# Optimization experiments

Measured on AMD Instinct MI355X. Metric: run time of the kernel, lower is better.

Reference implementation:

```python
import jax, jax.numpy as jnp
import numpy as np

D_MODEL = 1024
D_FF = 4096
N_EXPERTS = 8
TOP_K = 2

def setup_inputs() -> dict:
    key = jax.random.key(0)
    ks = jax.random.split(key, 8)
    s = 1.0 / np.sqrt(D_MODEL)
    sf = 1.0 / np.sqrt(D_FF)
    return {
        "x": jax.random.normal(ks[0], (4, 1024, D_MODEL), dtype=jnp.float32),
        "W1": jax.random.uniform(ks[1], (N_EXPERTS, D_MODEL, D_FF), jnp.float32, -s, s),
        "b1": jax.random.uniform(ks[2], (N_EXPERTS, D_FF), jnp.float32, -s, s),
        "W2": jax.random.uniform(ks[3], (N_EXPERTS, D_FF, D_MODEL), jnp.float32, -sf, sf),
        "b2": jax.random.uniform(ks[4], (N_EXPERTS, D_MODEL), jnp.float32, -sf, sf),
        "Wg": jax.random.uniform(ks[5], (D_MODEL, N_EXPERTS), jnp.float32, -s, s),
        "bg": jax.random.uniform(ks[6], (N_EXPERTS,), jnp.float32, -s, s),
    }

def reference(x, W1, b1, W2, b2, Wg, bg):
    # gate: [B,S,E]
    logits = jnp.einsum('bsd,de->bse', x, Wg) + bg
    probs = jax.nn.softmax(logits, axis=-1)
    # top-k mask + renormalize (k < n_experts)
    topk_vals, topk_idx = jax.lax.top_k(probs, TOP_K)
    mask = jax.nn.one_hot(topk_idx, N_EXPERTS, dtype=probs.dtype).sum(axis=-2)
    probs = probs * mask
    denom = probs.sum(axis=-1, keepdims=True)
    denom = denom + (denom == 0).astype(probs.dtype)
    probs = probs / denom
    # dense expert compute: all experts on all tokens. h: [B,E,S,d_ff]
    h = jnp.einsum('bsd,edf->besf', x, W1) + b1[None, :, None, :]
    h = jax.nn.gelu(h, approximate=False)
    y = jnp.einsum('besf,efd->besd', h, W2) + b2[None, :, None, :]
    # weighted combine over experts: [B,S,d]
    out = jnp.einsum('bse,besd->bsd', probs, y)
    return out
```

## Files before the change

### kernel.cpp

```cpp
#include <hip/hip_runtime.h>
#include <hip/hip_bf16.h>

#define NTOK   4096
#define DMODEL 1024
#define DFF    4096
#define NEXP   8
#define TOPK   2
#define BM 128
#define BN 128
#define BK 64
#define NSLOT   (NTOK*TOPK)
#define MAXSLOT (NSLOT + NEXP*BM)
#define MAXTILE (MAXSLOT/BM)

typedef __attribute__((ext_vector_type(8))) short bf16x8;
typedef __attribute__((ext_vector_type(8))) unsigned short u16x8;
typedef __attribute__((ext_vector_type(4))) float f32x4;

__device__ __forceinline__ unsigned short f2bf(float f){
    union { float f; unsigned int u; } v; v.f = f;
    unsigned int r = (v.u + 0x7fffu + ((v.u >> 16) & 1u)) >> 16;
    return (unsigned short)r;
}

__device__ __forceinline__ void gload16(const unsigned short* g, unsigned short* l){
    __builtin_amdgcn_global_load_lds(
        (const __attribute__((address_space(1))) void*)g,
        (__attribute__((address_space(3))) void*)l,
        16, 0, 0);
}

__global__ __launch_bounds__(256) void k_transpose_convert2(const float* __restrict__ W1,
                                                            const float* __restrict__ W2,
                                                            unsigned short* __restrict__ W1t,
                                                            unsigned short* __restrict__ W2t)
{
    __shared__ float tile[64][65];
    int z = blockIdx.z;
    const float* src; unsigned short* dst; int R, C, r0, c0;
    if(z < 8){
        src = W1  + (size_t)z * DMODEL * DFF;
        dst = W1t + (size_t)z * DMODEL * DFF;
        R = DMODEL; C = DFF;
        r0 = blockIdx.y * 64; c0 = blockIdx.x * 64;
    } else {
        src = W2  + (size_t)(z-8) * DFF * DMODEL;
        dst = W2t + (size_t)(z-8) * DFF * DMODEL;
        R = DFF; C = DMODEL;
        r0 = blockIdx.x * 64; c0 = blockIdx.y * 64;
    }
    int t = threadIdx.x;
    int tr  = t >> 4;
    int tc4 = (t & 15) * 4;
    #pragma unroll
    for(int i=0;i<4;i++){
        float4 v = *(const float4*)&src[(size_t)(r0 + tr + i*16)*C + c0 + tc4];
        tile[tc4+0][tr + i*16] = v.x;
        tile[tc4+1][tr + i*16] = v.y;
        tile[tc4+2][tr + i*16] = v.z;
        tile[tc4+3][tr + i*16] = v.w;
    }
    __syncthreads();
    int cr = t >> 3;
    int rb = (t & 7) * 8;
    #pragma unroll
    for(int i=0;i<2;i++){
        int c = cr + i*32;
        u16x8 o;
        #pragma unroll
        for(int q=0;q<8;q++) o[q] = f2bf(tile[c][rb + q]);
        *(u16x8*)&dst[(size_t)(c0 + c)*R + r0 + rb] = o;
    }
}

__global__ __launch_bounds__(256) void k_gate(const float* __restrict__ x,
                                              const float* __restrict__ Wg,
                                              const float* __restrict__ bg,
                                              unsigned short* __restrict__ Xb,
                                              float* __restrict__ out,
                                              int* __restrict__ token_e,
                                              float* __restrict__ token_w,
                                              int* __restrict__ cnt)
{
    int tid = threadIdx.x;
    const float4* xs = (const float4*)x + (size_t)blockIdx.x * 1024;
    ushort4* xd = (ushort4*)Xb + (size_t)blockIdx.x * 1024;
    float4* oz = (float4*)out + (size_t)blockIdx.x * 1024;
    float4 z4 = {0.f,0.f,0.f,0.f};
    #pragma unroll
    for(int rep=0;rep<4;rep++){
        float4 v = xs[rep*256 + tid];
        ushort4 o; o.x=f2bf(v.x); o.y=f2bf(v.y); o.z=f2bf(v.z); o.w=f2bf(v.w);
        xd[rep*256 + tid] = o;
        oz[rep*256 + tid] = z4;
    }

    int wid = tid >> 6, lane = tid & 63;
    int t = blockIdx.x * 4 + wid;
    const float* xr = x + (size_t)t * DMODEL;
    float pe[NEXP];
    #pragma unroll
    for(int e=0;e<NEXP;e++) pe[e] = 0.f;
    for(int i=0;i<DMODEL/64;i++){
        int d = i*64 + lane;
        float xv = xr[d];
        const float* wr = Wg + (size_t)d * NEXP;
        #pragma unroll
        for(int e=0;e<NEXP;e++) pe[e] += xv * wr[e];
    }
    #pragma unroll
    for(int off=32; off>0; off>>=1){
        #pragma unroll
        for(int e=0;e<NEXP;e++) pe[e] += __shfl_xor(pe[e], off);
    }
    if(lane == 0){
        float lg[NEXP], mx = -1e30f;
        #pragma unroll
        for(int e=0;e<NEXP;e++){ lg[e] = pe[e] + bg[e]; mx = fmaxf(mx, lg[e]); }
        float pr[NEXP];
        #pragma unroll
        for(int e=0;e<NEXP;e++) pr[e] = expf(lg[e] - mx);
        int e0 = 0; float p0 = pr[0];
        #pragma unroll
        for(int e=1;e<NEXP;e++) if(pr[e] > p0){ p0 = pr[e]; e0 = e; }
        int e1 = -1; float p1 = -1.f;
        #pragma unroll
        for(int e=0;e<NEXP;e++) if(e != e0 && pr[e] > p1){ p1 = pr[e]; e1 = e; }
        float dn = p0 + p1;
        token_e[2*t]   = e0; token_w[2*t]   = p0/dn;
        token_e[2*t+1] = e1; token_w[2*t+1] = p1/dn;
        atomicAdd(&cnt[e0], 1); atomicAdd(&cnt[e1], 1);
    }
}

__global__ __launch_bounds__(256) void k_prefix(const int* __restrict__ cnt,
                                                int* __restrict__ tile_e,
                                                int* __restrict__ tile_row0,
                                                int* __restrict__ tile_valid,
                                                int* __restrict__ cursor,
                                                int* __restrict__ slot_token)
{
    int tid = threadIdx.x;
    if(tid == 0){
        int off = 0, nt = 0;
        for(int e=0;e<NEXP;e++){
            cursor[e] = off;
            int c = cnt[e];
            for(int r=0;r<c;r+=BM){
                tile_e[nt] = e; tile_row0[nt] = off + r;
                tile_valid[nt] = (c - r < BM) ? (c - r) : BM;
                nt++;
            }
            off += ((c + BM - 1)/BM)*BM;
        }
        for(int i=nt;i<MAXTILE;i++){ tile_e[i]=0; tile_row0[i]=0; tile_valid[i]=0; }
    }
    for(int s=tid; s<MAXSLOT; s+=256) slot_token[s] = 0;
}

__global__ __launch_bounds__(256) void k_scatter(const int* __restrict__ token_e,
                                                 const float* __restrict__ token_w,
                                                 int* __restrict__ cursor,
                                                 int* __restrict__ slot_token,
                                                 float* __restrict__ slot_w)
{
    int i = blockIdx.x*256 + threadIdx.x;
    int e = token_e[i];
    int s = atomicAdd(&cursor[e], 1);
    slot_token[s] = i >> 1;
    slot_w[s] = token_w[i];
}

template<bool GATHER, bool GELU>
__global__ __launch_bounds__(256, 3) void k_gemm(const unsigned short* __restrict__ A,
                                                 const unsigned short* __restrict__ Bw,
                                                 const float* __restrict__ bias,
                                                 const int* __restrict__ tile_e,
                                                 const int* __restrict__ tile_row0,
                                                 const int* __restrict__ tile_valid,
                                                 const int* __restrict__ slot_token,
                                                 const float* __restrict__ slot_w,
                                                 unsigned short* __restrict__ OutH,
                                                 float* __restrict__ outF,
                                                 int K, int N)
{
    int xb = blockIdx.x;
    int tid = (xb & 7) * (MAXTILE/8) + (xb >> 3);
    int valid = tile_valid[tid];
    if(valid == 0) return;
    int e = tile_e[tid];
    int row0 = tile_row0[tid];
    int n0 = blockIdx.y * BN;
    const unsigned short* Be = Bw + (size_t)e * N * K;

    __shared__ unsigned short As[BM*BK];
    __shared__ unsigned short Bs[BN*BK];

    int t = threadIdx.x;
    int lane = t & 63;
    int wid = t >> 6;
    int wr = wid >> 1, wc = wid & 1;

    int srow = t >> 3;
    int csw  = (t & 7) ^ (srow & 7);
    const unsigned short* arow[4];
    const unsigned short* brow[4];
    #pragma unroll
    for(int i=0;i<4;i++){
        int r = i*32 + srow;
        size_t aoff;
        if(GATHER) aoff = (size_t)slot_token[row0 + r] * (size_t)K;
        else       aoff = (size_t)(row0 + r) * (size_t)K;
        arow[i] = A  + aoff + csw*8;
        brow[i] = Be + (size_t)(n0 + r)*K + csw*8;
    }
    unsigned short* alds = As + (size_t)t * 8;
    unsigned short* blds = Bs + (size_t)t * 8;

    f32x4 acc[4][4];
    #pragma unroll
    for(int m=0;m<4;m++)
        #pragma unroll
        for(int n=0;n<4;n++)
            acc[m][n] = (f32x4){0.f,0.f,0.f,0.f};

    int rl = lane & 15;
    int g  = lane >> 4;
    int rx = rl & 7;

    for(int k0=0;k0<K;k0+=BK){
        __syncthreads();
        #pragma unroll
        for(int i=0;i<4;i++){
            gload16(arow[i] + k0, alds + i*2048);
            gload16(brow[i] + k0, blds + i*2048);
        }
        __syncthreads();

        #pragma unroll
        for(int kb=0;kb<2;kb++){
            int sw = ((kb*4 + g) ^ rx) * 8;
            bf16x8 af[4], bfv[4];
            #pragma unroll
            for(int m=0;m<4;m++) af[m]  = *(const bf16x8*)&As[(wr*64 + m*16 + rl)*BK + sw];
            #pragma unroll
            for(int n=0;n<4;n++) bfv[n] = *(const bf16x8*)&Bs[(wc*64 + n*16 + rl)*BK + sw];
            #pragma unroll
            for(int m=0;m<4;m++)
                #pragma unroll
                for(int n=0;n<4;n++)
                    acc[m][n] = __builtin_amdgcn_mfma_f32_16x16x32_bf16(af[m], bfv[n], acc[m][n], 0, 0, 0);
        }
    }

    const float* be = bias + (size_t)e * N;
    #pragma unroll
    for(int m=0;m<4;m++){
        int rb = wr*64 + m*16 + g*4;
        #pragma unroll
        for(int j=0;j<4;j++){
            int r = rb + j;
            if(r >= valid) continue;
            size_t grow = (size_t)(row0 + r);
            if(GELU){
                #pragma unroll
                for(int n=0;n<4;n++){
                    int col = n0 + wc*64 + n*16 + rl;
                    float v = acc[m][n][j] + be[col];
                    v = 0.5f * v * (1.f + erff(v * 0.70710678118654752f));
                    OutH[grow * (size_t)N + col] = f2bf(v);
                }
            } else {
                float wsc = slot_w[grow];
                float* orow = outF + (size_t)slot_token[grow] * DMODEL;
                #pragma unroll
                for(int n=0;n<4;n++){
                    int col = n0 + wc*64 + n*16 + rl;
                    float v = (acc[m][n][j] + be[col]) * wsc;
                    atomicAdd(&orow[col], v);
                }
            }
        }
    }
}

extern "C" void kernel_launch(void* const* d_in, const int* in_sizes, int n_in,
                              void* d_out, int out_size, void* d_ws, size_t ws_size,
                              hipStream_t stream)
{
    const float* x  = (const float*)d_in[0];
    const float* W1 = (const float*)d_in[1];
    const float* b1 = (const float*)d_in[2];
    const float* W2 = (const float*)d_in[3];
    const float* b2 = (const float*)d_in[4];
    const float* Wg = (const float*)d_in[5];
    const float* bg = (const float*)d_in[6];
    float* out = (float*)d_out;

    char* p = (char*)d_ws;
    auto alloc = [&](size_t bytes)->char*{
        char* r = p; p += (bytes + 255) & ~(size_t)255; return r;
    };
    unsigned short* W1t = (unsigned short*)alloc((size_t)NEXP*DFF*DMODEL*2);
    unsigned short* W2t = (unsigned short*)alloc((size_t)NEXP*DMODEL*DFF*2);
    unsigned short* Xb  = (unsigned short*)alloc((size_t)NTOK*DMODEL*2);
    unsigned short* H   = (unsigned short*)alloc((size_t)MAXSLOT*DFF*2);
    int*   slot_token = (int*)alloc(MAXSLOT*4);
    float* slot_w     = (float*)alloc(MAXSLOT*4);
    int*   token_e    = (int*)alloc(NSLOT*4);
    float* token_w    = (float*)alloc(NSLOT*4);
    int*   cnt        = (int*)alloc(64);
    int*   cursor     = (int*)alloc(64);
    int*   tile_e     = (int*)alloc(MAXTILE*4);
    int*   tile_row0  = (int*)alloc(MAXTILE*4);
    int*   tile_valid = (int*)alloc(MAXTILE*4);
    (void)ws_size; (void)in_sizes; (void)n_in; (void)out_size;

    hipMemsetAsync(cnt, 0, 64, stream);
    k_gate<<<NTOK/4, 256, 0, stream>>>(x, Wg, bg, Xb, out, token_e, token_w, cnt);
    k_transpose_convert2<<<dim3(DFF/64, DMODEL/64, 16), 256, 0, stream>>>(W1, W2, W1t, W2t);
    k_prefix<<<1, 256, 0, stream>>>(cnt, tile_e, tile_row0, tile_valid, cursor, slot_token);
    k_scatter<<<NSLOT/256, 256, 0, stream>>>(token_e, token_w, cursor, slot_token, slot_w);
    k_gemm<true, true ><<<dim3(MAXTILE, DFF/BN), 256, 0, stream>>>(
        Xb, W1t, b1, tile_e, tile_row0, tile_valid, slot_token, slot_w, H, nullptr,
        DMODEL, DFF);
    k_gemm<false,false><<<dim3(MAXTILE, DMODEL/BN), 256, 0, stream>>>(
        H,  W2t, b2, tile_e, tile_row0, tile_valid, slot_token, slot_w, nullptr, out,
        DFF, DMODEL);
}
```

Measured before the change: 481.0 us.

## Overlap weight transpose-convert with gating and first GEMM via extra blocks

Removes the standalone weight transpose kernel. The W1 transpose now runs in two-thirds of the blocks of the gating kernel, and the W2 transpose runs in every fifth y-column of blocks in the first GEMM launch. The goal is to hide the bandwidth-bound fp32-to-bf16 conversion behind the gate and GEMM compute instead of serialising it. The risks are contention between the two kinds of work inside one launch and an uneven mix of block types, and the second GEMM still depends on W2t being complete when the first kernel ends.

```diff
diff --git a/kernel.cpp b/kernel.cpp
--- a/kernel.cpp
+++ b/kernel.cpp
@@ -12,6 +12,7 @@
 #define NSLOT   (NTOK*TOPK)
 #define MAXSLOT (NSLOT + NEXP*BM)
 #define MAXTILE (MAXSLOT/BM)
+#define NWTILE  8192
 
 typedef __attribute__((ext_vector_type(8))) short bf16x8;
 typedef __attribute__((ext_vector_type(8))) unsigned short u16x8;
@@ -30,25 +31,11 @@
         16, 0, 0);
 }
 
-__global__ __launch_bounds__(256) void k_transpose_convert2(const float* __restrict__ W1,
-                                                            const float* __restrict__ W2,
-                                                            unsigned short* __restrict__ W1t,
-                                                            unsigned short* __restrict__ W2t)
-{
-    __shared__ float tile[64][65];
-    int z = blockIdx.z;
-    const float* src; unsigned short* dst; int R, C, r0, c0;
-    if(z < 8){
-        src = W1  + (size_t)z * DMODEL * DFF;
-        dst = W1t + (size_t)z * DMODEL * DFF;
-        R = DMODEL; C = DFF;
-        r0 = blockIdx.y * 64; c0 = blockIdx.x * 64;
-    } else {
-        src = W2  + (size_t)(z-8) * DFF * DMODEL;
-        dst = W2t + (size_t)(z-8) * DFF * DMODEL;
-        R = DFF; C = DMODEL;
-        r0 = blockIdx.x * 64; c0 = blockIdx.y * 64;
-    }
+__device__ __forceinline__ void transpose_tile64(const float* __restrict__ src,
+                                                 unsigned short* __restrict__ dst,
+                                                 int R, int C, int r0, int c0,
+                                                 float (*tile)[65])
+{
     int t = threadIdx.x;
     int tr  = t >> 4;
     int tc4 = (t & 15) * 4;
@@ -71,21 +58,39 @@
         for(int q=0;q<8;q++) o[q] = f2bf(tile[c][rb + q]);
         *(u16x8*)&dst[(size_t)(c0 + c)*R + r0 + rb] = o;
     }
-}
-
-__global__ __launch_bounds__(256) void k_gate(const float* __restrict__ x,
-                                              const float* __restrict__ Wg,
-                                              const float* __restrict__ bg,
-                                              unsigned short* __restrict__ Xb,
-                                              float* __restrict__ out,
-                                              int* __restrict__ token_e,
-                                              float* __restrict__ token_w,
-                                              int* __restrict__ cnt)
-{
+    __syncthreads();
+}
+
+__global__ __launch_bounds__(256) void k_gate_w1t(const float* __restrict__ x,
+                                                  const float* __restrict__ Wg,
+                                                  const float* __restrict__ bg,
+                                                  const float* __restrict__ W1,
+                                                  unsigned short* __restrict__ Xb,
+                                                  unsigned short* __restrict__ W1t,
+                                                  float* __restrict__ out,
+                                                  int* __restrict__ token_e,
+                                                  float* __restrict__ token_w,
+                                                  int* __restrict__ cnt)
+{
+    __shared__ float tile[64][65];
+    int bx = blockIdx.x;
+    if(bx % 3 != 0){
+        int w = bx - bx/3 - 1;
+        for(int t2 = w; t2 < NWTILE; t2 += 2048){
+            int z  = t2 >> 10;
+            int rem = t2 & 1023;
+            int rt = rem >> 6;
+            int ct = rem & 63;
+            transpose_tile64(W1 + (size_t)z*DMODEL*DFF, W1t + (size_t)z*DMODEL*DFF,
+                             DMODEL, DFF, rt*64, ct*64, tile);
+        }
+        return;
+    }
+    int b = bx / 3;
     int tid = threadIdx.x;
-    const float4* xs = (const float4*)x + (size_t)blockIdx.x * 1024;
-    ushort4* xd = (ushort4*)Xb + (size_t)blockIdx.x * 1024;
-    float4* oz = (float4*)out + (size_t)blockIdx.x * 1024;
+    const float4* xs = (const float4*)x + (size_t)b * 1024;
+    ushort4* xd = (ushort4*)Xb + (size_t)b * 1024;
+    float4* oz = (float4*)out + (size_t)b * 1024;
     float4 z4 = {0.f,0.f,0.f,0.f};
     #pragma unroll
     for(int rep=0;rep<4;rep++){
@@ -96,7 +101,7 @@
     }
 
     int wid = tid >> 6, lane = tid & 63;
-    int t = blockIdx.x * 4 + wid;
+    int t = b * 4 + wid;
     const float* xr = x + (size_t)t * DMODEL;
     float pe[NEXP];
     #pragma unroll
@@ -171,7 +176,7 @@
     slot_w[s] = token_w[i];
 }
 
-template<bool GATHER, bool GELU>
+template<bool GATHER, bool GELU, bool FUSET>
 __global__ __launch_bounds__(256, 3) void k_gemm(const unsigned short* __restrict__ A,
                                                  const unsigned short* __restrict__ Bw,
                                                  const float* __restrict__ bias,
@@ -182,19 +187,37 @@
                                                  const float* __restrict__ slot_w,
                                                  unsigned short* __restrict__ OutH,
                                                  float* __restrict__ outF,
+                                                 const float* __restrict__ Wsrc,
+                                                 unsigned short* __restrict__ Wdst,
                                                  int K, int N)
 {
+    __shared__ __align__(16) unsigned short SM[BM*BK + BN*BK];
+    unsigned short* As = SM;
+    unsigned short* Bs = SM + BM*BK;
+
+    int y = blockIdx.y;
+    if(FUSET && ((y+1) % 5) == 0){
+        float (*tile)[65] = (float(*)[65])SM;
+        int w = blockIdx.x * 8 + (y/5);
+        for(int t2 = w; t2 < NWTILE; t2 += 576){
+            int z  = t2 >> 10;
+            int rem = t2 & 1023;
+            int rt = rem >> 4;
+            int ct = rem & 15;
+            transpose_tile64(Wsrc + (size_t)z*DFF*DMODEL, Wdst + (size_t)z*DFF*DMODEL,
+                             DFF, DMODEL, rt*64, ct*64, tile);
+        }
+        return;
+    }
+
     int xb = blockIdx.x;
     int tid = (xb & 7) * (MAXTILE/8) + (xb >> 3);
     int valid = tile_valid[tid];
     if(valid == 0) return;
     int e = tile_e[tid];
     int row0 = tile_row0[tid];
-    int n0 = blockIdx.y * BN;
+    int n0 = (FUSET ? (y - (y+1)/5) : y) * BN;
     const unsigned short* Be = Bw + (size_t)e * N * K;
-
-    __shared__ unsigned short As[BM*BK];
-    __shared__ unsigned short Bs[BN*BK];
 
     int t = threadIdx.x;
     int lane = t & 63;
@@ -317,14 +340,14 @@
     (void)ws_size; (void)in_sizes; (void)n_in; (void)out_size;
 
     hipMemsetAsync(cnt, 0, 64, stream);
-    k_gate<<<NTOK/4, 256, 0, stream>>>(x, Wg, bg, Xb, out, token_e, token_w, cnt);
-    k_transpose_convert2<<<dim3(DFF/64, DMODEL/64, 16), 256, 0, stream>>>(W1, W2, W1t, W2t);
+    k_gate_w1t<<<3072, 256, 0, stream>>>(x, Wg, bg, W1, Xb, W1t, out,
+                                         token_e, token_w, cnt);
     k_prefix<<<1, 256, 0, stream>>>(cnt, tile_e, tile_row0, tile_valid, cursor, slot_token);
     k_scatter<<<NSLOT/256, 256, 0, stream>>>(token_e, token_w, cursor, slot_token, slot_w);
-    k_gemm<true, true ><<<dim3(MAXTILE, DFF/BN), 256, 0, stream>>>(
+    k_gemm<true, true, true ><<<dim3(MAXTILE, 40), 256, 0, stream>>>(
         Xb, W1t, b1, tile_e, tile_row0, tile_valid, slot_token, slot_w, H, nullptr,
-        DMODEL, DFF);
-    k_gemm<false,false><<<dim3(MAXTILE, DMODEL/BN), 256, 0, stream>>>(
+        W2, W2t, DMODEL, DFF);
+    k_gemm<false,false,false><<<dim3(MAXTILE, DMODEL/BN), 256, 0, stream>>>(
         H,  W2t, b2, tile_e, tile_row0, tile_valid, slot_token, slot_w, nullptr, out,
-        DFF, DMODEL);
-}
+        nullptr, nullptr, DFF, DMODEL);
+}
```

Measured after the change: 429.0 us (median of 3 runs). 1.12x faster.
